# Optimization experiments

Measured on AMD Instinct MI355X. Metric: run time of the kernel, lower is better.

The kernel has to match this reference:

```python
import jax, jax.numpy as jnp
import numpy as np


def _edge_index(B, N, T):
    # Fully-connected graph minus self loops within each (sample, timestep) block of N nodes.
    ii, jj = np.meshgrid(np.arange(N), np.arange(N), indexing='ij')
    mask = ii != jj
    ei = ii[mask].astype(np.int32)  # [N*(N-1)] source within block
    ej = jj[mask].astype(np.int32)  # [N*(N-1)] target within block
    offs = (np.arange(B * T, dtype=np.int32) * N)[:, None]  # block offsets
    row = (ei[None, :] + offs).reshape(-1)
    col = (ej[None, :] + offs).reshape(-1)
    return jnp.asarray(row), jnp.asarray(col)


def setup_inputs() -> dict:
    key = jax.random.key(0)
    k1, k2, k3 = jax.random.split(key, 3)
    B, N, T, F, E = 32, 64, 50, 2, 8
    x = jax.random.normal(k1, (B, N, T, F), dtype=jnp.float32)
    W_res = jax.random.normal(k2, (F, E), dtype=jnp.float32) / np.sqrt(F)
    W_gcn = jax.random.normal(k3, (F, E), dtype=jnp.float32) / np.sqrt(F)
    b_gcn = jnp.zeros((E,), dtype=jnp.float32)
    return {"x": x, "W_res": W_res, "W_gcn": W_gcn, "b_gcn": b_gcn}


def reference(x, W_res, W_gcn, b_gcn):
    B, N, T, F = x.shape
    E = W_gcn.shape[1]
    M = B * T * N
    # preprocess: [B,N,T,F] -> swap -> [B,T,N,F] -> flatten nodes [M,F]
    nodes = x.transpose(0, 2, 1, 3).reshape(M, F)
    row, col = _edge_index(B, N, T)
    # distance edge weights: w = min(1/||xi-xj||, 1), zero distance -> 1e-6
    delta = nodes[row] - nodes[col]  # [E_tot, F]
    dist = jnp.linalg.norm(delta, axis=1)
    dist = jnp.where(dist == 0.0, jnp.float32(1e-6), dist)
    w = jnp.minimum(1.0 / dist, 1.0)
    # GCNConv normalization with self loops (weight 1.0)
    deg = jax.ops.segment_sum(w, col, num_segments=M) + 1.0
    dinv = deg ** -0.5
    norm = dinv[row] * w * dinv[col]
    h = nodes @ W_gcn  # [M, E]
    agg = jax.ops.segment_sum(norm[:, None] * h[row], col, num_segments=M)
    agg = agg + (dinv * dinv)[:, None] * h  # self-loop contribution
    enc = agg + b_gcn
    # residual linear (no bias) + relu
    enc = jax.nn.relu(enc + nodes @ W_res)
    # postprocess: [M,E] -> [B,T,N,E], select agent 0 -> [B,T,E]
    enc_sp = enc.reshape(B, T, N, E)[:, :, 0, :]
    inputs = x[:, 0]  # [B, T, F]
    return inputs, enc_sp
```

## Files before the change

kernel.cpp:

```cpp
#include <hip/hip_runtime.h>


__global__ __launch_bounds__(64) void encoder_spatial_kernel(
    const float* __restrict__ x,
    const float* __restrict__ W_res,
    const float* __restrict__ W_gcn,
    const float* __restrict__ b_gcn,
    float* __restrict__ out)
{
    constexpr int N = 64, T = 50, F = 2, E = 8;
    const int g    = blockIdx.x;
    const int b    = g / T;
    const int t    = g % T;
    const int lane = threadIdx.x;

    const float2 p = *reinterpret_cast<const float2*>(
        x + ((size_t)(b * N + lane) * T + t) * F);

    __shared__ float2 sp[64];
    sp[lane] = p;
    __syncthreads();

    float deg = 0.0f;
    float w0  = 0.0f;
    #pragma unroll
    for (int k = 0; k < 64; ++k) {
        const float2 q = sp[k];
        const float dx = p.x - q.x;
        const float dy = p.y - q.y;
        const float d2 = dx * dx + dy * dy;
        const float w = fminf(__builtin_amdgcn_rsqf(d2), 1.0f);
        deg += w;
        if (k == 0) w0 = w;
    }
    const float dinv = __builtin_amdgcn_rsqf(deg);

    const float c = (lane == 0) ? 0.0f : dinv * w0;
    float cx = c * p.x;
    float cy = c * p.y;
    #pragma unroll
    for (int off = 32; off > 0; off >>= 1) {
        cx += __shfl_xor(cx, off, 64);
        cy += __shfl_xor(cy, off, 64);
    }

    const float dinv0 = __shfl(dinv, 0, 64);
    const float px0 = sp[0].x;
    const float py0 = sp[0].y;

    if (lane < E) {
        const int e = lane;
        const float wg0 = W_gcn[e];
        const float wg1 = W_gcn[E + e];
        float agg = dinv0 * (cx * wg0 + cy * wg1)
                  + dinv0 * dinv0 * (px0 * wg0 + py0 * wg1);
        float enc = agg + b_gcn[e] + px0 * W_res[e] + py0 * W_res[E + e];
        out[3200 + g * E + e] = fmaxf(enc, 0.0f);
    }
    if (lane < F) {
        out[g * F + lane] = (lane == 0) ? px0 : py0;
    }
}

extern "C" void kernel_launch(void* const* d_in, const int* in_sizes, int n_in,
                              void* d_out, int out_size, void* d_ws, size_t ws_size,
                              hipStream_t stream) {
    const float* x     = (const float*)d_in[0];
    const float* W_res = (const float*)d_in[1];
    const float* W_gcn = (const float*)d_in[2];
    const float* b_gcn = (const float*)d_in[3];
    float* out = (float*)d_out;

    encoder_spatial_kernel<<<32 * 50, 64, 0, stream>>>(x, W_res, W_gcn, b_gcn, out);
}
```

Before: 9.693 us.

## Process eight timestep groups per 512-thread block with coalesced shared staging

Each block now handles eight (batch, timestep) groups with 512 threads instead of one group per 64-thread block. The load is remapped so consecutive threads read consecutive timesteps, which are adjacent in memory, and results are staged in a padded shared array. The degree accumulation is also split into four independent partial sums to shorten the dependency chain. This reduces block count and launch overhead and improves load coalescing, but leaves only 200 blocks, which may underfill the GPU's compute units.

```diff
diff --git a/kernel.cpp b/kernel.cpp
--- a/kernel.cpp
+++ b/kernel.cpp
@@ -1,7 +1,7 @@
 #include <hip/hip_runtime.h>
 
 
-__global__ __launch_bounds__(64) void encoder_spatial_kernel(
+__global__ __launch_bounds__(512) void encoder_spatial_kernel(
     const float* __restrict__ x,
     const float* __restrict__ W_res,
     const float* __restrict__ W_gcn,
@@ -9,30 +9,46 @@
     float* __restrict__ out)
 {
     constexpr int N = 64, T = 50, F = 2, E = 8;
-    const int g    = blockIdx.x;
-    const int b    = g / T;
-    const int t    = g % T;
-    const int lane = threadIdx.x;
+    const int g0 = blockIdx.x * 8;
 
-    const float2 p = *reinterpret_cast<const float2*>(
-        x + ((size_t)(b * N + lane) * T + t) * F);
+    __shared__ float2 sp[8][65];
 
-    __shared__ float2 sp[64];
-    sp[lane] = p;
+    {
+        const int i = threadIdx.x;
+        const int n = i >> 3;
+        const int j = i & 7;
+        const int g = g0 + j;
+        const int b = g / T;
+        const int t = g % T;
+        sp[j][n] = *reinterpret_cast<const float2*>(
+            x + ((size_t)(b * N + n) * T + t) * F);
+    }
     __syncthreads();
 
-    float deg = 0.0f;
-    float w0  = 0.0f;
+    const int j    = threadIdx.x >> 6;
+    const int lane = threadIdx.x & 63;
+    const int g    = g0 + j;
+
+    const float2 p = sp[j][lane];
+
+    float d0 = 0.f, d1 = 0.f, d2a = 0.f, d3 = 0.f;
+    float w0 = 0.f;
     #pragma unroll
-    for (int k = 0; k < 64; ++k) {
-        const float2 q = sp[k];
-        const float dx = p.x - q.x;
-        const float dy = p.y - q.y;
-        const float d2 = dx * dx + dy * dy;
-        const float w = fminf(__builtin_amdgcn_rsqf(d2), 1.0f);
-        deg += w;
-        if (k == 0) w0 = w;
+    for (int k = 0; k < 64; k += 4) {
+        #pragma unroll
+        for (int u = 0; u < 4; ++u) {
+            const float2 q = sp[j][k + u];
+            const float dx = p.x - q.x;
+            const float dy = p.y - q.y;
+            const float w  = fminf(__builtin_amdgcn_rsqf(dx * dx + dy * dy), 1.0f);
+            if (k + u == 0) { w0 = w; d0 += w; }
+            else if (u == 0) d0 += w;
+            else if (u == 1) d1 += w;
+            else if (u == 2) d2a += w;
+            else             d3 += w;
+        }
     }
+    const float deg  = (d0 + d1) + (d2a + d3);
     const float dinv = __builtin_amdgcn_rsqf(deg);
 
     const float c = (lane == 0) ? 0.0f : dinv * w0;
@@ -45,17 +61,16 @@
     }
 
     const float dinv0 = __shfl(dinv, 0, 64);
-    const float px0 = sp[0].x;
-    const float py0 = sp[0].y;
+    const float px0 = sp[j][0].x;
+    const float py0 = sp[j][0].y;
 
     if (lane < E) {
-        const int e = lane;
-        const float wg0 = W_gcn[e];
-        const float wg1 = W_gcn[E + e];
+        const float wg0 = W_gcn[lane];
+        const float wg1 = W_gcn[E + lane];
         float agg = dinv0 * (cx * wg0 + cy * wg1)
                   + dinv0 * dinv0 * (px0 * wg0 + py0 * wg1);
-        float enc = agg + b_gcn[e] + px0 * W_res[e] + py0 * W_res[E + e];
-        out[3200 + g * E + e] = fmaxf(enc, 0.0f);
+        float enc = agg + b_gcn[lane] + px0 * W_res[lane] + py0 * W_res[E + lane];
+        out[3200 + g * E + lane] = fmaxf(enc, 0.0f);
     }
     if (lane < F) {
         out[g * F + lane] = (lane == 0) ? px0 : py0;
@@ -71,5 +86,5 @@
     const float* b_gcn = (const float*)d_in[3];
     float* out = (float*)d_out;
 
-    encoder_spatial_kernel<<<32 * 50, 64, 0, stream>>>(x, W_res, W_gcn, b_gcn, out);
+    encoder_spatial_kernel<<<200, 512, 0, stream>>>(x, W_res, W_gcn, b_gcn, out);
 }
```

New measurement: 9.647 us. About the same (-0.5%).
